# Optimization experiments

Hardware: AMD Instinct MI355X
Metric: run time of the kernel (lower is better)

## Reference

```python
import jax, jax.numpy as jnp
import numpy as np

SCALE = 8.0  # cfg.TEST_SCALE (eval path)


def setup_inputs() -> dict:
    key = jax.random.key(0)
    ks = jax.random.split(key, 5)
    N, D, F, NC = 65536, 1024, 300, 81
    return {
        "x": jax.random.normal(ks[0], (N, D), dtype=jnp.float32),
        "W_cls": jax.random.normal(ks[1], (1, D), dtype=jnp.float32) * 0.01,
        "b_cls": jnp.zeros((1,), dtype=jnp.float32),
        "W_sem": jax.random.normal(ks[2], (F, D), dtype=jnp.float32) * 0.01,
        "b_sem": jnp.zeros((F,), dtype=jnp.float32),
        "W_bbox": jax.random.normal(ks[3], (NC * 4, D), dtype=jnp.float32) * 0.001,
        "b_bbox": jnp.zeros((NC * 4,), dtype=jnp.float32),
        "sem_matrix": jax.random.normal(ks[4], (NC - 1, F), dtype=jnp.float32),
    }


def reference(x, W_cls, b_cls, W_sem, b_sem, W_bbox, b_bbox, sem_matrix):
    # b_score: Linear(D, 1)
    b_score = x @ W_cls.T + b_cls                      # [N, 1]
    # sem: Linear(D, F)
    sem = x @ W_sem.T + b_sem                          # [N, F]
    # eval path: scale * L2-row-normalized semantic matrix
    sm = SCALE * sem_matrix / jnp.linalg.norm(sem_matrix, axis=1, keepdims=True)
    # the original per-class repeat/mul/sum loop == one GEMM
    cls_score = sem @ sm.T                             # [N, NC-1]
    scores = jnp.concatenate([b_score, cls_score], axis=1)  # [N, NC]
    bbox_deltas = x @ W_bbox.T + b_bbox                # [N, NC*4]
    return (scores, bbox_deltas)
```

## Files before the change

kernel.cpp:

```cpp
#include <hip/hip_runtime.h>
#include <hip/hip_bf16.h>
#include <stdint.h>

#define KDIM 1024
#define NPAD 512
#define NCOLS 405
#define SCORE_COLS 81
#define BBOX_COLS 324
#define NROWS 65536
#define FDIM 300

typedef short v8s __attribute__((ext_vector_type(8)));
typedef float v4f __attribute__((ext_vector_type(4)));

typedef __attribute__((address_space(3))) uint32_t lds_u32_t;
typedef __attribute__((address_space(1))) uint32_t glb_u32_t;

__device__ __forceinline__ void async16(void* lds, const void* g) {
    __builtin_amdgcn_global_load_lds((const glb_u32_t*)g, (lds_u32_t*)lds, 16, 0, 0);
}

__device__ __forceinline__ uint16_t f2bf(float f) {
    union { float f; uint32_t u; } c; c.f = f;
    uint32_t r = c.u + 0x7FFFu + ((c.u >> 16) & 1u);
    return (uint16_t)(r >> 16);
}

__global__ void fill_w(const float* __restrict__ Wcls, const float* __restrict__ bcls,
                       const float* __restrict__ Wbbox, const float* __restrict__ bbbox,
                       uint16_t* __restrict__ Wt, float* __restrict__ bt) {
    int idx = blockIdx.x * 256 + threadIdx.x;
    int row = idx >> 10, k = idx & 1023;
    if (!(row >= 1 && row < 1 + 80)) {
        float v;
        if (row == 0) v = Wcls[k];
        else if (row < 81 + BBOX_COLS) v = Wbbox[(size_t)(row - 81) * KDIM + k];
        else v = 0.f;
        Wt[idx] = f2bf(v);
    }
    if (k == 0 && !(row >= 1 && row < 81)) {
        float b;
        if (row == 0) b = bcls[0];
        else if (row < 81 + BBOX_COLS) b = bbbox[row - 81];
        else b = 0.f;
        bt[row] = b;
    }
}

__global__ void fill_w_sem(const float* __restrict__ Wsem, const float* __restrict__ bsem,
                           const float* __restrict__ semm,
                           uint16_t* __restrict__ Wt, float* __restrict__ bt) {
    const int n = blockIdx.x;
    const int kq = blockIdx.y;
    const int tid = threadIdx.x;
    __shared__ float s_row[FDIM];
    __shared__ float red[256];
    __shared__ float s_scale, s_bdot;

    const float* sr = semm + (size_t)n * FDIM;
    float p = 0.f, pb = 0.f;
    for (int f = tid; f < FDIM; f += 256) {
        float v = sr[f];
        s_row[f] = v;
        p += v * v;
        pb += v * bsem[f];
    }
    red[tid] = p; __syncthreads();
    for (int s = 128; s > 0; s >>= 1) { if (tid < s) red[tid] += red[tid + s]; __syncthreads(); }
    float norm2 = red[0]; __syncthreads();
    red[tid] = pb; __syncthreads();
    for (int s = 128; s > 0; s >>= 1) { if (tid < s) red[tid] += red[tid + s]; __syncthreads(); }
    if (tid == 0) { s_scale = 8.0f / sqrtf(norm2); s_bdot = red[0]; }
    __syncthreads();
    const float scale = s_scale;
    if (kq == 0 && tid == 0) bt[1 + n] = scale * s_bdot;

    const int k = kq * 256 + tid;
    float acc = 0.f;
    #pragma unroll 8
    for (int f = 0; f < FDIM; ++f) acc += s_row[f] * Wsem[(size_t)f * KDIM + k];
    Wt[(size_t)(1 + n) * KDIM + k] = f2bf(scale * acc);
}

__device__ __forceinline__ void compute_tile(const uint16_t* As, const uint16_t* Bs,
                                             int wr, int wc, int l16, int quad,
                                             v4f acc[4][4]) {
    v8s a[4], b[4];
    #pragma unroll
    for (int mi = 0; mi < 4; ++mi)
        a[mi] = *(const v8s*)&As[(wr * 64 + mi * 16 + l16) * 32 + quad * 8];
    #pragma unroll
    for (int ni = 0; ni < 4; ++ni)
        b[ni] = *(const v8s*)&Bs[(wc * 64 + ni * 16 + l16) * 32 + quad * 8];
    #pragma unroll
    for (int mi = 0; mi < 4; ++mi)
        #pragma unroll
        for (int ni = 0; ni < 4; ++ni)
            acc[mi][ni] = __builtin_amdgcn_mfma_f32_16x16x32_bf16(a[mi], b[ni], acc[mi][ni], 0, 0, 0);
}

__global__ __launch_bounds__(256, 2) void gemm_fused(
        const float* __restrict__ x, const uint16_t* __restrict__ Wt,
        const float* __restrict__ bt, float* __restrict__ out) {
    const int tid = threadIdx.x;
    const int wave = tid >> 6, lane = tid & 63;
    const int wr = wave & 1, wc = wave >> 1;
    const int quad = lane >> 4, l16 = lane & 15;
    const int ntile = blockIdx.x, mtile = blockIdx.y;

    __shared__ __align__(16) uint16_t As[2][128 * 32];
    __shared__ __align__(16) uint16_t Bs[2][128 * 32];

    const float*    xb = x  + (size_t)mtile * 128 * KDIM;
    const uint16_t* wb = Wt + (size_t)ntile * 128 * KDIM;

    const int colbase = ntile * 128 + wc * 64;
    float bias[4];
    #pragma unroll
    for (int ni = 0; ni < 4; ++ni) bias[ni] = bt[colbase + ni * 16 + l16];

    v4f acc[4][4];
    #pragma unroll
    for (int mi = 0; mi < 4; ++mi)
        #pragma unroll
        for (int ni = 0; ni < 4; ++ni)
            acc[mi][ni] = v4f{0.f, 0.f, 0.f, 0.f};

    float4 av[4];
    #pragma unroll
    for (int i = 0; i < 2; ++i) {
        int c = i * 256 + tid, nr = c >> 2, kc = c & 3;
        async16(&Bs[0][c * 8], wb + (size_t)nr * KDIM + kc * 8);
    }
    #pragma unroll
    for (int i = 0; i < 4; ++i) {
        int c = i * 256 + tid, m = c >> 3, kc = c & 7;
        av[i] = *(const float4*)(xb + (size_t)m * KDIM + kc * 4);
    }
    #pragma unroll
    for (int i = 0; i < 4; ++i) {
        int c = i * 256 + tid, m = c >> 3, kc = c & 7;
        __hip_bfloat162 lo = __float22bfloat162_rn(make_float2(av[i].x, av[i].y));
        __hip_bfloat162 hi = __float22bfloat162_rn(make_float2(av[i].z, av[i].w));
        uint2 p; p.x = *(uint32_t*)&lo; p.y = *(uint32_t*)&hi;
        *(uint2*)&As[0][m * 32 + kc * 4] = p;
    }

    #pragma unroll 2
    for (int kt = 0; kt < 31; ++kt) {
        const int buf = kt & 1;
        __syncthreads();
        #pragma unroll
        for (int i = 0; i < 2; ++i) {
            int c = i * 256 + tid, nr = c >> 2, kc = c & 3;
            async16(&Bs[buf ^ 1][c * 8], wb + (size_t)nr * KDIM + (kt + 1) * 32 + kc * 8);
        }
        #pragma unroll
        for (int i = 0; i < 4; ++i) {
            int c = i * 256 + tid, m = c >> 3, kc = c & 7;
            av[i] = *(const float4*)(xb + (size_t)m * KDIM + (kt + 1) * 32 + kc * 4);
        }
        compute_tile(As[buf], Bs[buf], wr, wc, l16, quad, acc);
        #pragma unroll
        for (int i = 0; i < 4; ++i) {
            int c = i * 256 + tid, m = c >> 3, kc = c & 7;
            __hip_bfloat162 lo = __float22bfloat162_rn(make_float2(av[i].x, av[i].y));
            __hip_bfloat162 hi = __float22bfloat162_rn(make_float2(av[i].z, av[i].w));
            uint2 p; p.x = *(uint32_t*)&lo; p.y = *(uint32_t*)&hi;
            *(uint2*)&As[buf ^ 1][m * 32 + kc * 4] = p;
        }
    }
    __syncthreads();
    compute_tile(As[1], Bs[1], wr, wc, l16, quad, acc);

    const int rowbase = mtile * 128 + wr * 64;
    #pragma unroll
    for (int ni = 0; ni < 4; ++ni) {
        const int c = colbase + ni * 16 + l16;
        if (c < NCOLS) {
            #pragma unroll
            for (int mi = 0; mi < 4; ++mi)
                #pragma unroll
                for (int r = 0; r < 4; ++r) {
                    int row = rowbase + mi * 16 + quad * 4 + r;
                    float v = acc[mi][ni][r] + bias[ni];
                    if (c < SCORE_COLS)
                        out[(size_t)row * SCORE_COLS + c] = v;
                    else
                        out[(size_t)NROWS * SCORE_COLS + (size_t)row * BBOX_COLS + (c - SCORE_COLS)] = v;
                }
        }
    }
}

extern "C" void kernel_launch(void* const* d_in, const int* in_sizes, int n_in,
                              void* d_out, int out_size, void* d_ws, size_t ws_size,
                              hipStream_t stream) {
    const float* x     = (const float*)d_in[0];
    const float* Wcls  = (const float*)d_in[1];
    const float* bcls  = (const float*)d_in[2];
    const float* Wsem  = (const float*)d_in[3];
    const float* bsem  = (const float*)d_in[4];
    const float* Wbbox = (const float*)d_in[5];
    const float* bbbox = (const float*)d_in[6];
    const float* semm  = (const float*)d_in[7];
    float* out = (float*)d_out;

    uint16_t* Wt = (uint16_t*)d_ws;
    float*    bt = (float*)((char*)d_ws + (size_t)NPAD * KDIM * 2);

    fill_w<<<dim3(2048), dim3(256), 0, stream>>>(Wcls, bcls, Wbbox, bbbox, Wt, bt);
    fill_w_sem<<<dim3(80, 4), dim3(256), 0, stream>>>(Wsem, bsem, semm, Wt, bt);
    gemm_fused<<<dim3(4, 512), dim3(256), 0, stream>>>(x, Wt, bt, out);
}
```

Measured before the change: 573.1 us.

## Compute all output columns per block to read x once, stage epilogue via LDS

The GEMM is retiled so each 512-thread block handles a 64-row M tile across all 512 padded N columns. Previously x was reloaded and reconverted to bf16 by four N-tile blocks; now it is read once. The weight matrix is stored in a k-tile-major layout so each k-step's B slice is one contiguous copy, and the A tile gets a padded LDS stride. The epilogue stages results through LDS so global stores are coalesced row-contiguous writes, at the cost of larger LDS use (about 70KB per block), which limits occupancy.

```diff
diff --git a/kernel.cpp b/kernel.cpp
--- a/kernel.cpp
+++ b/kernel.cpp
@@ -10,6 +10,7 @@
 #define NROWS 65536
 #define FDIM 300
 
+
 typedef short v8s __attribute__((ext_vector_type(8)));
 typedef float v4f __attribute__((ext_vector_type(4)));
 
@@ -24,6 +25,10 @@
     union { float f; uint32_t u; } c; c.f = f;
     uint32_t r = c.u + 0x7FFFu + ((c.u >> 16) & 1u);
     return (uint16_t)(r >> 16);
+}
+
+__device__ __forceinline__ size_t wt_off(int row, int k) {
+    return (size_t)(k >> 5) * (NPAD * 32) + (size_t)row * 32 + (k & 31);
 }
 
 __global__ void fill_w(const float* __restrict__ Wcls, const float* __restrict__ bcls,
@@ -31,12 +36,12 @@
                        uint16_t* __restrict__ Wt, float* __restrict__ bt) {
     int idx = blockIdx.x * 256 + threadIdx.x;
     int row = idx >> 10, k = idx & 1023;
-    if (!(row >= 1 && row < 1 + 80)) {
+    if (!(row >= 1 && row < 81)) {
         float v;
         if (row == 0) v = Wcls[k];
         else if (row < 81 + BBOX_COLS) v = Wbbox[(size_t)(row - 81) * KDIM + k];
         else v = 0.f;
-        Wt[idx] = f2bf(v);
+        Wt[wt_off(row, k)] = f2bf(v);
     }
     if (k == 0 && !(row >= 1 && row < 81)) {
         float b;
@@ -79,16 +84,21 @@
     float acc = 0.f;
     #pragma unroll 8
     for (int f = 0; f < FDIM; ++f) acc += s_row[f] * Wsem[(size_t)f * KDIM + k];
-    Wt[(size_t)(1 + n) * KDIM + k] = f2bf(scale * acc);
-}
+    Wt[wt_off(1 + n, k)] = f2bf(scale * acc);
+}
+
+#define A_STRIDE 36
+#define A_BUF_ELEMS (64 * A_STRIDE)
+#define B_BUF_ELEMS (NPAD * 32)
+#define SMEM_BYTES (2 * A_BUF_ELEMS * 2 + 2 * B_BUF_ELEMS * 2)
 
 __device__ __forceinline__ void compute_tile(const uint16_t* As, const uint16_t* Bs,
-                                             int wr, int wc, int l16, int quad,
+                                             int wc, int l16, int quad,
                                              v4f acc[4][4]) {
     v8s a[4], b[4];
     #pragma unroll
     for (int mi = 0; mi < 4; ++mi)
-        a[mi] = *(const v8s*)&As[(wr * 64 + mi * 16 + l16) * 32 + quad * 8];
+        a[mi] = *(const v8s*)&As[(mi * 16 + l16) * A_STRIDE + quad * 8];
     #pragma unroll
     for (int ni = 0; ni < 4; ++ni)
         b[ni] = *(const v8s*)&Bs[(wc * 64 + ni * 16 + l16) * 32 + quad * 8];
@@ -99,22 +109,22 @@
             acc[mi][ni] = __builtin_amdgcn_mfma_f32_16x16x32_bf16(a[mi], b[ni], acc[mi][ni], 0, 0, 0);
 }
 
-__global__ __launch_bounds__(256, 2) void gemm_fused(
+__global__ __launch_bounds__(512, 4) void gemm_fused(
         const float* __restrict__ x, const uint16_t* __restrict__ Wt,
         const float* __restrict__ bt, float* __restrict__ out) {
     const int tid = threadIdx.x;
     const int wave = tid >> 6, lane = tid & 63;
-    const int wr = wave & 1, wc = wave >> 1;
+    const int wc = wave;
     const int quad = lane >> 4, l16 = lane & 15;
-    const int ntile = blockIdx.x, mtile = blockIdx.y;
-
-    __shared__ __align__(16) uint16_t As[2][128 * 32];
-    __shared__ __align__(16) uint16_t Bs[2][128 * 32];
-
-    const float*    xb = x  + (size_t)mtile * 128 * KDIM;
-    const uint16_t* wb = Wt + (size_t)ntile * 128 * KDIM;
-
-    const int colbase = ntile * 128 + wc * 64;
+    const int mtile = blockIdx.x;
+
+    __shared__ __align__(16) char smem[SMEM_BYTES];
+    uint16_t* As = (uint16_t*)smem;
+    uint16_t* Bs = (uint16_t*)(smem + 2 * A_BUF_ELEMS * 2);
+
+    const float* xb = x + (size_t)mtile * 64 * KDIM;
+
+    const int colbase = wc * 64;
     float bias[4];
     #pragma unroll
     for (int ni = 0; ni < 4; ++ni) bias[ni] = bt[colbase + ni * 16 + l16];
@@ -126,69 +136,71 @@
         for (int ni = 0; ni < 4; ++ni)
             acc[mi][ni] = v4f{0.f, 0.f, 0.f, 0.f};
 
-    float4 av[4];
-    #pragma unroll
-    for (int i = 0; i < 2; ++i) {
-        int c = i * 256 + tid, nr = c >> 2, kc = c & 3;
-        async16(&Bs[0][c * 8], wb + (size_t)nr * KDIM + kc * 8);
-    }
+    const int am = tid >> 3, akc = tid & 7;
+    float4 av;
+
     #pragma unroll
     for (int i = 0; i < 4; ++i) {
-        int c = i * 256 + tid, m = c >> 3, kc = c & 7;
-        av[i] = *(const float4*)(xb + (size_t)m * KDIM + kc * 4);
-    }
-    #pragma unroll
-    for (int i = 0; i < 4; ++i) {
-        int c = i * 256 + tid, m = c >> 3, kc = c & 7;
-        __hip_bfloat162 lo = __float22bfloat162_rn(make_float2(av[i].x, av[i].y));
-        __hip_bfloat162 hi = __float22bfloat162_rn(make_float2(av[i].z, av[i].w));
+        int c = i * 512 + tid;
+        async16(&Bs[0 * B_BUF_ELEMS + c * 8], Wt + (size_t)c * 8);
+    }
+    av = *(const float4*)(xb + (size_t)am * KDIM + akc * 4);
+    {
+        __hip_bfloat162 lo = __float22bfloat162_rn(make_float2(av.x, av.y));
+        __hip_bfloat162 hi = __float22bfloat162_rn(make_float2(av.z, av.w));
         uint2 p; p.x = *(uint32_t*)&lo; p.y = *(uint32_t*)&hi;
-        *(uint2*)&As[0][m * 32 + kc * 4] = p;
-    }
-
-    #pragma unroll 2
+        *(uint2*)&As[0 * A_BUF_ELEMS + am * A_STRIDE + akc * 4] = p;
+    }
+
     for (int kt = 0; kt < 31; ++kt) {
         const int buf = kt & 1;
         __syncthreads();
         #pragma unroll
-        for (int i = 0; i < 2; ++i) {
-            int c = i * 256 + tid, nr = c >> 2, kc = c & 3;
-            async16(&Bs[buf ^ 1][c * 8], wb + (size_t)nr * KDIM + (kt + 1) * 32 + kc * 8);
-        }
-        #pragma unroll
         for (int i = 0; i < 4; ++i) {
-            int c = i * 256 + tid, m = c >> 3, kc = c & 7;
-            av[i] = *(const float4*)(xb + (size_t)m * KDIM + (kt + 1) * 32 + kc * 4);
-        }
-        compute_tile(As[buf], Bs[buf], wr, wc, l16, quad, acc);
-        #pragma unroll
-        for (int i = 0; i < 4; ++i) {
-            int c = i * 256 + tid, m = c >> 3, kc = c & 7;
-            __hip_bfloat162 lo = __float22bfloat162_rn(make_float2(av[i].x, av[i].y));
-            __hip_bfloat162 hi = __float22bfloat162_rn(make_float2(av[i].z, av[i].w));
+            int c = i * 512 + tid;
+            async16(&Bs[(buf ^ 1) * B_BUF_ELEMS + c * 8],
+                    Wt + (size_t)(kt + 1) * B_BUF_ELEMS + (size_t)c * 8);
+        }
+        av = *(const float4*)(xb + (size_t)am * KDIM + (kt + 1) * 32 + akc * 4);
+        compute_tile(&As[buf * A_BUF_ELEMS], &Bs[buf * B_BUF_ELEMS], wc, l16, quad, acc);
+        {
+            __hip_bfloat162 lo = __float22bfloat162_rn(make_float2(av.x, av.y));
+            __hip_bfloat162 hi = __float22bfloat162_rn(make_float2(av.z, av.w));
             uint2 p; p.x = *(uint32_t*)&lo; p.y = *(uint32_t*)&hi;
-            *(uint2*)&As[buf ^ 1][m * 32 + kc * 4] = p;
+            *(uint2*)&As[(buf ^ 1) * A_BUF_ELEMS + am * A_STRIDE + akc * 4] = p;
         }
     }
     __syncthreads();
-    compute_tile(As[1], Bs[1], wr, wc, l16, quad, acc);
-
-    const int rowbase = mtile * 128 + wr * 64;
-    #pragma unroll
-    for (int ni = 0; ni < 4; ++ni) {
-        const int c = colbase + ni * 16 + l16;
-        if (c < NCOLS) {
+    compute_tile(&As[1 * A_BUF_ELEMS], &Bs[1 * B_BUF_ELEMS], wc, l16, quad, acc);
+
+    const int rowbase = mtile * 64;
+    float* eps = (float*)smem;
+    float* outb = out + (size_t)NROWS * SCORE_COLS;
+    #pragma unroll
+    for (int h = 0; h < 2; ++h) {
+        __syncthreads();
+        #pragma unroll
+        for (int mi2 = 0; mi2 < 2; ++mi2) {
+            const int mi = h * 2 + mi2;
             #pragma unroll
-            for (int mi = 0; mi < 4; ++mi)
-                #pragma unroll
-                for (int r = 0; r < 4; ++r) {
-                    int row = rowbase + mi * 16 + quad * 4 + r;
-                    float v = acc[mi][ni][r] + bias[ni];
-                    if (c < SCORE_COLS)
-                        out[(size_t)row * SCORE_COLS + c] = v;
-                    else
-                        out[(size_t)NROWS * SCORE_COLS + (size_t)row * BBOX_COLS + (c - SCORE_COLS)] = v;
+            for (int ni = 0; ni < 4; ++ni) {
+                const int col = colbase + ni * 16 + l16;
+                if (col < NCOLS) {
+                    #pragma unroll
+                    for (int r = 0; r < 4; ++r)
+                        eps[(mi2 * 16 + quad * 4 + r) * 409 + col] = acc[mi][ni][r] + bias[ni];
                 }
+            }
+        }
+        __syncthreads();
+        const int row0 = rowbase + h * 32;
+        for (int idx = tid; idx < 32 * SCORE_COLS; idx += 512) {
+            int r = idx / SCORE_COLS, c = idx - r * SCORE_COLS;
+            out[(size_t)(row0 + r) * SCORE_COLS + c] = eps[r * 409 + c];
+        }
+        for (int idx = tid; idx < 32 * BBOX_COLS; idx += 512) {
+            int r = idx / BBOX_COLS, c = idx - r * BBOX_COLS;
+            outb[(size_t)(row0 + r) * BBOX_COLS + c] = eps[r * 409 + SCORE_COLS + c];
         }
     }
 }
@@ -211,5 +223,5 @@
 
     fill_w<<<dim3(2048), dim3(256), 0, stream>>>(Wcls, bcls, Wbbox, bbbox, Wt, bt);
     fill_w_sem<<<dim3(80, 4), dim3(256), 0, stream>>>(Wsem, bsem, semm, Wt, bt);
-    gemm_fused<<<dim3(4, 512), dim3(256), 0, stream>>>(x, Wt, bt, out);
-}
+    gemm_fused<<<dim3(1024), dim3(512), 0, stream>>>(x, Wt, bt, out);
+}
```

Result: faster. 524.9 us (-8.4%).
